# Kernel tuning notes

Hardware: AMD Instinct MI355X
Metric: run time of the kernel (lower is better)

## Reference

```python
import jax, jax.numpy as jnp
import numpy as np

DIM = 10  # GMM components == feature dim


def _conv(x, w, b):
    y = jax.lax.conv_general_dilated(x, w, window_strides=(1, 1), padding='VALID',
                                     dimension_numbers=('NCHW', 'OIHW', 'NCHW'))
    return y + b[None, :, None, None]


def _gmm(x, centers, raw_mats):
    # x: [B, d]; centers: [K, d]; raw_mats: [K, d, d] with K == d == DIM
    K, d = centers.shape
    I = jnp.eye(d, dtype=x.dtype)
    L = jnp.tril(raw_mats, -1) + I                       # unit lower-triangular [K,d,d]
    root_D = jnp.diagonal(raw_mats, axis1=-2, axis2=-1)  # [K,d]
    D = root_D * root_D + 1e-4
    # Sigma_inv = L^{-T} D^{-1} L^{-1}
    L_inv = jax.scipy.linalg.solve_triangular(L, jnp.broadcast_to(I, L.shape), lower=True)
    Sigma_inv = jnp.einsum('kai,ka,kaj->kij', L_inv, 1.0 / D, L_inv)
    det_scale = jax.lax.rsqrt(jnp.prod(D, axis=-1))      # [K]
    diff = x[:, None, :] - centers[None, :, :]           # [B,K,d]
    dist_sq = jnp.einsum('bkd,kde,bke->bk', diff, Sigma_inv, diff)
    expo = -0.5 * dist_sq
    expo_safe = expo - jnp.max(expo, axis=1, keepdims=True)
    numer = det_scale[None, :] * jnp.exp(expo_safe)
    return numer / jnp.sum(numer, axis=1, keepdims=True)


def setup_inputs() -> dict:
    key = jax.random.key(0)
    ks = jax.random.split(key, 12)
    B = 4096
    x = jax.random.normal(ks[0], (B, 1, 28, 28), dtype=jnp.float32)
    conv1_w = jax.random.normal(ks[1], (32, 1, 3, 3), jnp.float32) * (1.0 / np.sqrt(1 * 9))
    conv1_b = jnp.zeros((32,), jnp.float32)
    conv2_w = jax.random.normal(ks[2], (64, 32, 3, 3), jnp.float32) * (1.0 / np.sqrt(32 * 9))
    conv2_b = jnp.zeros((64,), jnp.float32)
    fc1_w = jax.random.normal(ks[3], (128, 9216), jnp.float32) * (1.0 / np.sqrt(9216))
    fc1_b = jnp.zeros((128,), jnp.float32)
    fc2_w = jax.random.normal(ks[4], (DIM, 128), jnp.float32) * (1.0 / np.sqrt(128))
    fc2_b = jnp.zeros((DIM,), jnp.float32)
    centers = jax.random.normal(ks[5], (DIM, DIM), jnp.float32)
    raw_mats = jax.random.normal(ks[6], (DIM, DIM, DIM), jnp.float32) * 0.1 + jnp.eye(DIM)[None]
    return {'x': x, 'conv1_w': conv1_w, 'conv1_b': conv1_b, 'conv2_w': conv2_w,
            'conv2_b': conv2_b, 'fc1_w': fc1_w, 'fc1_b': fc1_b, 'fc2_w': fc2_w,
            'fc2_b': fc2_b, 'centers': centers, 'raw_mats': raw_mats}


def reference(x, conv1_w, conv1_b, conv2_w, conv2_b, fc1_w, fc1_b, fc2_w, fc2_b, centers, raw_mats):
    h = jax.nn.relu(_conv(x, conv1_w, conv1_b))          # [B,32,26,26]
    h = jax.nn.relu(_conv(h, conv2_w, conv2_b))          # [B,64,24,24]
    h = jax.lax.reduce_window(h, -jnp.inf, jax.lax.max, (1, 1, 2, 2), (1, 1, 2, 2), 'VALID')
    h = h.reshape(h.shape[0], -1)                        # [B,9216] (dropout = identity in eval)
    h = jax.nn.relu(h @ fc1_w.T + fc1_b)
    h = h @ fc2_w.T + fc2_b                              # [B,10]
    return _gmm(h, centers, raw_mats)
```

## Files before the change

kernel.cpp:

```cpp
#include <hip/hip_runtime.h>

typedef _Float16 half_t;
typedef _Float16 half8  __attribute__((ext_vector_type(8)));
typedef _Float16 half2v __attribute__((ext_vector_type(2)));
typedef float    floatx4 __attribute__((ext_vector_type(4)));

#define MFMA16(a, b, c) __builtin_amdgcn_mfma_f32_16x16x32_f16((a), (b), (c), 0, 0, 0)

__global__ void k_prep(const float* __restrict__ fw1, half_t* __restrict__ W1h,
                       const float* __restrict__ w2, half_t* __restrict__ W2T,
                       const float* __restrict__ raw, float* __restrict__ Sinv,
                       float* __restrict__ dets) {
    const int blk = blockIdx.x;
    const int t = threadIdx.x;
    if (blk < 4608) {
        const int i = blk * 256 + t;
        W1h[i] = (half_t)fw1[i];
    } else if (blk < 4680) {
        const int i = (blk - 4608) * 256 + t;
        if (i < 18432) {
            const int tap = i / 2048;
            const int r = i - tap * 2048;
            const int co = r >> 5;
            const int ci = r & 31;
            W2T[i] = (half_t)w2[(co * 32 + ci) * 9 + tap];
        }
    } else if (t < 10) {
        const float* R = raw + t * 100;
        float Rr[100];
#pragma unroll
        for (int i = 0; i < 100; ++i) Rr[i] = R[i];
        float Li[10][10];
#pragma unroll
        for (int j = 0; j < 10; ++j) {
#pragma unroll
            for (int i = 0; i < 10; ++i) Li[i][j] = (i == j) ? 1.0f : 0.0f;
#pragma unroll
            for (int i = 1; i < 10; ++i) {
                if (i > j) {
                    float s = 0.0f;
#pragma unroll
                    for (int m = 0; m < 10; ++m)
                        if (m >= j && m < i) s -= Rr[i * 10 + m] * Li[m][j];
                    Li[i][j] = s;
                }
            }
        }
        float Dl[10];
        float prod = 1.0f;
#pragma unroll
        for (int a = 0; a < 10; ++a) {
            float rd = Rr[a * 10 + a];
            float dv = rd * rd + 1e-4f;
            Dl[a] = 1.0f / dv;
            prod *= dv;
        }
        dets[t] = rsqrtf(prod);
#pragma unroll
        for (int i = 0; i < 10; ++i)
#pragma unroll
            for (int j = 0; j < 10; ++j) {
                float s = 0.0f;
#pragma unroll
                for (int a = 0; a < 10; ++a) s += Li[a][i] * Dl[a] * Li[a][j];
                Sinv[t * 100 + i * 10 + j] = s;
            }
    }
}

__global__ __launch_bounds__(256, 2) void k_convs(
    const float* __restrict__ x, const float* __restrict__ w1,
    const float* __restrict__ b1, const float* __restrict__ b2,
    const half_t* __restrict__ W2T, half_t* __restrict__ h2p) {
    __shared__ float s_x[784];
    __shared__ float s_w1[288];
    __shared__ float s_b1[32];
    __shared__ float s_b2[64];
    __shared__ __align__(16) half_t s_h1[4][26][26][8];

    const int t = threadIdx.x;
    const int b = blockIdx.x;

    for (int i = t; i < 784; i += 256) s_x[i] = x[(size_t)b * 784 + i];
    for (int i = t; i < 288; i += 256) s_w1[i] = w1[i];
    if (t < 32) s_b1[t] = b1[t];
    if (t < 64) s_b2[t] = b2[t];
    __syncthreads();

    const int w = t >> 6;
    const int ln = t & 63;
    const int n16 = ln & 15;
    const int q = ln >> 4;

    {
        float wr[8][9], br[8];
#pragma unroll
        for (int j = 0; j < 8; ++j) {
            br[j] = s_b1[w * 8 + j];
#pragma unroll
            for (int k = 0; k < 9; ++k) wr[j][k] = s_w1[(w * 8 + j) * 9 + k];
        }
        for (int p = ln; p < 676; p += 64) {
            const int yy = p / 26;
            const int xx = p - yy * 26;
            float win[9];
#pragma unroll
            for (int r = 0; r < 3; ++r)
#pragma unroll
                for (int c = 0; c < 3; ++c) win[r * 3 + c] = s_x[(yy + r) * 28 + xx + c];
            half8 hv;
#pragma unroll
            for (int j = 0; j < 8; ++j) {
                float a = br[j];
#pragma unroll
                for (int k = 0; k < 9; ++k) a = fmaf(win[k], wr[j][k], a);
                hv[j] = (half_t)fmaxf(a, 0.0f);
            }
            *(half8*)(&s_h1[w][yy][xx][0]) = hv;
        }
    }

    half8 bf[9][4];
#pragma unroll
    for (int tap = 0; tap < 9; ++tap)
#pragma unroll
        for (int ct = 0; ct < 4; ++ct)
            bf[tap][ct] = *(const half8*)(W2T + ((tap * 64 + ct * 16 + n16) * 32 + q * 8));

    __syncthreads();

#pragma unroll
    for (int tap = 0; tap < 9; ++tap)
#pragma unroll
        for (int ct = 0; ct < 4; ++ct)
            asm volatile("" : "+v"(bf[tap][ct]));

    const int dy = (ln >> 3) & 1;
    const int dx = ln & 7;

    for (int i = 0; i < 9; ++i) {
        const int mt = w * 9 + i;
        const int ty = mt / 3;
        const int tx = mt - ty * 3;
        const int y0 = 2 * ty, x0 = 8 * tx;
        floatx4 acc[4];
#pragma unroll
        for (int ct = 0; ct < 4; ++ct) acc[ct] = (floatx4){0.f, 0.f, 0.f, 0.f};
#pragma unroll
        for (int tap = 0; tap < 9; ++tap) {
            const int ky = tap / 3;
            const int kx = tap - ky * 3;
            half8 af = *(const half8*)(&s_h1[q][y0 + dy + ky][x0 + dx + kx][0]);
#pragma unroll
            for (int ct = 0; ct < 4; ++ct) acc[ct] = MFMA16(af, bf[tap][ct], acc[ct]);
        }
#pragma unroll
        for (int ct = 0; ct < 4; ++ct) {
            float p0 = fmaxf(acc[ct][0], acc[ct][1]);
            float p1 = fmaxf(acc[ct][2], acc[ct][3]);
            p0 = fmaxf(p0, __shfl_xor(p0, 32, 64));
            p1 = fmaxf(p1, __shfl_xor(p1, 32, 64));
            if (q < 2) {
                const int co = ct * 16 + n16;
                const float bb = s_b2[co];
                half2v hz;
                hz[0] = (half_t)fmaxf(p0 + bb, 0.0f);
                hz[1] = (half_t)fmaxf(p1 + bb, 0.0f);
                *(half2v*)(h2p + (size_t)b * 9216 + co * 144 + ty * 12 + 4 * tx + 2 * q) = hz;
            }
        }
    }
}

__global__ __launch_bounds__(256) void k_fc1(const half_t* __restrict__ A,
                                             const half_t* __restrict__ W,
                                             half_t* __restrict__ part) {
    const int t = threadIdx.x;
    const int mb = blockIdx.x;
    const int kb = blockIdx.y;
    const int w = t >> 6, ln = t & 63, n16 = ln & 15, q = ln >> 4;

    const half_t* a0 = A + (size_t)(mb * 128 + w * 32 + n16) * 9216 + kb * 576 + q * 8;
    const half_t* a1 = a0 + (size_t)16 * 9216;
    const half_t* wp = W + (size_t)n16 * 9216 + kb * 576 + q * 8;

    floatx4 acc[2][8];
#pragma unroll
    for (int s = 0; s < 2; ++s)
#pragma unroll
        for (int nt = 0; nt < 8; ++nt) acc[s][nt] = (floatx4){0.f, 0.f, 0.f, 0.f};

    for (int kt = 0; kt < 18; ++kt) {
        const int ko = kt * 32;
        half8 af0 = *(const half8*)(a0 + ko);
        half8 af1 = *(const half8*)(a1 + ko);
#pragma unroll
        for (int nt = 0; nt < 8; ++nt) {
            half8 bfr = *(const half8*)(wp + (size_t)nt * 16 * 9216 + ko);
            acc[0][nt] = MFMA16(af0, bfr, acc[0][nt]);
            acc[1][nt] = MFMA16(af1, bfr, acc[1][nt]);
        }
    }
    const int rowbase = mb * 128 + w * 32;
#pragma unroll
    for (int s = 0; s < 2; ++s)
#pragma unroll
        for (int nt = 0; nt < 8; ++nt)
#pragma unroll
            for (int r = 0; r < 4; ++r) {
                const int row = rowbase + s * 16 + q * 4 + r;
                const int col = nt * 16 + n16;
                part[(size_t)kb * 524288 + (size_t)row * 128 + col] = (half_t)acc[s][nt][r];
            }
}

__global__ void k_fc1red(const half_t* __restrict__ part, const float* __restrict__ b,
                         half_t* __restrict__ h3) {
    const int idx = blockIdx.x * 256 + threadIdx.x;
    const int col = idx & 127;
    float s = 0.0f;
#pragma unroll
    for (int j = 0; j < 16; ++j) s += (float)part[(size_t)j * 524288 + idx];
    s = fmaxf(s + b[col], 0.0f);
    h3[idx] = (half_t)s;
}

__global__ __launch_bounds__(256) void k_fc2gmm(
    const half_t* __restrict__ h3, const float* __restrict__ fw,
    const float* __restrict__ fb, const float* __restrict__ cent,
    const float* __restrict__ Sinv, const float* __restrict__ dets,
    float* __restrict__ out) {
    __shared__ float sw[1280];
    __shared__ float sb[10];
    __shared__ float sc[100];
    __shared__ float ss[1000];
    __shared__ float sd[10];
    const int t = threadIdx.x;
    for (int i = t; i < 1280; i += 256) sw[i] = fw[i];
    if (t < 10) sb[t] = fb[t];
    if (t < 100) sc[t] = cent[t];
    for (int i = t; i < 1000; i += 256) ss[i] = Sinv[i];
    if (t < 10) sd[t] = dets[t];
    __syncthreads();

    const int bidx = blockIdx.x * 256 + t;
    half2v hh[64];
    const half2v* hp = (const half2v*)(h3 + (size_t)bidx * 128);
#pragma unroll
    for (int i = 0; i < 64; ++i) hh[i] = hp[i];

    float y[10];
#pragma unroll
    for (int o = 0; o < 10; ++o) {
        float a = sb[o];
#pragma unroll
        for (int k = 0; k < 64; ++k) {
            a = fmaf((float)hh[k][0], sw[o * 128 + 2 * k], a);
            a = fmaf((float)hh[k][1], sw[o * 128 + 2 * k + 1], a);
        }
        y[o] = a;
    }

    float expo[10];
    float mx = -3.402823466e38f;
#pragma unroll
    for (int k = 0; k < 10; ++k) {
        float d[10];
#pragma unroll
        for (int j = 0; j < 10; ++j) d[j] = y[j] - sc[k * 10 + j];
        float s = 0.0f;
#pragma unroll
        for (int i = 0; i < 10; ++i) {
            float r = 0.0f;
#pragma unroll
            for (int j = 0; j < 10; ++j) r = fmaf(ss[k * 100 + i * 10 + j], d[j], r);
            s = fmaf(d[i], r, s);
        }
        expo[k] = -0.5f * s;
        mx = fmaxf(mx, expo[k]);
    }
    float num[10];
    float sum = 0.0f;
#pragma unroll
    for (int k = 0; k < 10; ++k) {
        num[k] = sd[k] * __expf(expo[k] - mx);
        sum += num[k];
    }
    const float inv = 1.0f / sum;
#pragma unroll
    for (int k = 0; k < 10; ++k) out[(size_t)bidx * 10 + k] = num[k] * inv;
}

extern "C" void kernel_launch(void* const* d_in, const int* in_sizes, int n_in,
                              void* d_out, int out_size, void* d_ws, size_t ws_size,
                              hipStream_t stream) {
    const float* x = (const float*)d_in[0];
    const float* w1 = (const float*)d_in[1];
    const float* b1 = (const float*)d_in[2];
    const float* w2 = (const float*)d_in[3];
    const float* b2 = (const float*)d_in[4];
    const float* fw1 = (const float*)d_in[5];
    const float* fb1 = (const float*)d_in[6];
    const float* fw2 = (const float*)d_in[7];
    const float* fb2 = (const float*)d_in[8];
    const float* cen = (const float*)d_in[9];
    const float* raw = (const float*)d_in[10];
    float* out = (float*)d_out;

    char* ws = (char*)d_ws;
    half_t* W2T = (half_t*)(ws);
    half_t* W1h = (half_t*)(ws + 36864);
    half_t* h2p = (half_t*)(ws + 2396160);
    half_t* part = (half_t*)(ws + 77893632);
    half_t* h3h = (half_t*)(ws + 94670848);
    float* gS = (float*)(ws + 95719424);
    float* gD = (float*)(ws + 95723424);

    k_prep<<<4681, 256, 0, stream>>>(fw1, W1h, w2, W2T, raw, gS, gD);
    k_convs<<<4096, 256, 0, stream>>>(x, w1, b1, b2, W2T, h2p);
    k_fc1<<<dim3(32, 16), 256, 0, stream>>>(h2p, W1h, part);
    k_fc1red<<<2048, 256, 0, stream>>>(part, fb1, h3h);
    k_fc2gmm<<<16, 256, 0, stream>>>(h3h, fw2, fb2, cen, gS, gD, out);
}
```

Baseline: 283.6 us.

## Swizzle conv1 LDS layout, split conv2 channels across waves, parallelize GMM prep

The conv1 output in LDS becomes pixel-major with an XOR swizzle to reduce bank conflicts. Conv2 now splits output channels across wave pairs, so each wave holds half the B fragments. The M-tile mapping is changed so the 2x2 pool fits inside one accumulator's four elements, which removes the cross-lane shuffle. Launch bounds rise to 3 blocks per CU. The GMM precompute now spreads the triangular solve and Sigma_inv product over 100+ threads via shared memory instead of 10 serial threads. Output stores become scalar half writes, which may hurt coalescing.

Measured after the change: 261.2 us. 7.9% less time.

```diff
diff --git a/kernel.cpp b/kernel.cpp
--- a/kernel.cpp
+++ b/kernel.cpp
@@ -11,6 +11,9 @@
                        const float* __restrict__ w2, half_t* __restrict__ W2T,
                        const float* __restrict__ raw, float* __restrict__ Sinv,
                        float* __restrict__ dets) {
+    __shared__ float s_raw[1000];
+    __shared__ float s_Li[1000];
+    __shared__ float s_Dinv[100];
     const int blk = blockIdx.x;
     const int t = threadIdx.x;
     if (blk < 4608) {
@@ -25,50 +28,52 @@
             const int ci = r & 31;
             W2T[i] = (half_t)w2[(co * 32 + ci) * 9 + tap];
         }
-    } else if (t < 10) {
-        const float* R = raw + t * 100;
-        float Rr[100];
-#pragma unroll
-        for (int i = 0; i < 100; ++i) Rr[i] = R[i];
-        float Li[10][10];
-#pragma unroll
-        for (int j = 0; j < 10; ++j) {
-#pragma unroll
-            for (int i = 0; i < 10; ++i) Li[i][j] = (i == j) ? 1.0f : 0.0f;
-#pragma unroll
-            for (int i = 1; i < 10; ++i) {
-                if (i > j) {
-                    float s = 0.0f;
-#pragma unroll
-                    for (int m = 0; m < 10; ++m)
-                        if (m >= j && m < i) s -= Rr[i * 10 + m] * Li[m][j];
-                    Li[i][j] = s;
-                }
+    } else {
+        for (int i = t; i < 1000; i += 256) s_raw[i] = raw[i];
+        __syncthreads();
+        if (t < 100) {
+            const int k = t / 10;
+            const int j = t - k * 10;
+            float v[10];
+#pragma unroll
+            for (int i = 0; i < 10; ++i) {
+                float s = (i == j) ? 1.0f : 0.0f;
+#pragma unroll
+                for (int mm = 0; mm < 10; ++mm)
+                    if (mm < i) s -= s_raw[k * 100 + i * 10 + mm] * v[mm];
+                v[i] = s;
             }
-        }
-        float Dl[10];
-        float prod = 1.0f;
-#pragma unroll
-        for (int a = 0; a < 10; ++a) {
-            float rd = Rr[a * 10 + a];
-            float dv = rd * rd + 1e-4f;
-            Dl[a] = 1.0f / dv;
-            prod *= dv;
-        }
-        dets[t] = rsqrtf(prod);
-#pragma unroll
-        for (int i = 0; i < 10; ++i)
-#pragma unroll
-            for (int j = 0; j < 10; ++j) {
-                float s = 0.0f;
-#pragma unroll
-                for (int a = 0; a < 10; ++a) s += Li[a][i] * Dl[a] * Li[a][j];
-                Sinv[t * 100 + i * 10 + j] = s;
+#pragma unroll
+            for (int a = 0; a < 10; ++a) s_Li[k * 100 + a * 10 + j] = v[a];
+        } else if (t < 110) {
+            const int k = t - 100;
+            float prod = 1.0f;
+#pragma unroll
+            for (int a = 0; a < 10; ++a) {
+                const float rd = s_raw[k * 100 + a * 10 + a];
+                const float dv = rd * rd + 1e-4f;
+                s_Dinv[k * 10 + a] = 1.0f / dv;
+                prod *= dv;
             }
-    }
-}
-
-__global__ __launch_bounds__(256, 2) void k_convs(
+            dets[k] = rsqrtf(prod);
+        }
+        __syncthreads();
+        for (int idx = t; idx < 1000; idx += 256) {
+            const int k = idx / 100;
+            const int r = idx - k * 100;
+            const int ii = r / 10;
+            const int jj = r - ii * 10;
+            float s = 0.0f;
+#pragma unroll
+            for (int a = 0; a < 10; ++a)
+                s += s_Li[k * 100 + a * 10 + ii] * s_Dinv[k * 10 + a] *
+                     s_Li[k * 100 + a * 10 + jj];
+            Sinv[idx] = s;
+        }
+    }
+}
+
+__global__ __launch_bounds__(256, 3) void k_convs(
     const float* __restrict__ x, const float* __restrict__ w1,
     const float* __restrict__ b1, const float* __restrict__ b2,
     const half_t* __restrict__ W2T, half_t* __restrict__ h2p) {
@@ -76,7 +81,7 @@
     __shared__ float s_w1[288];
     __shared__ float s_b1[32];
     __shared__ float s_b2[64];
-    __shared__ __align__(16) half_t s_h1[4][26][26][8];
+    __shared__ __align__(16) half_t s_h1[21632];
 
     const int t = threadIdx.x;
     const int b = blockIdx.x;
@@ -116,59 +121,62 @@
                 for (int k = 0; k < 9; ++k) a = fmaf(win[k], wr[j][k], a);
                 hv[j] = (half_t)fmaxf(a, 0.0f);
             }
-            *(half8*)(&s_h1[w][yy][xx][0]) = hv;
-        }
-    }
-
-    half8 bf[9][4];
+            const int off = ((p << 6) + (w << 4)) ^ ((p & 7) << 4);
+            *(half8*)((char*)s_h1 + off) = hv;
+        }
+    }
+
+    const int cp = w & 1;
+    half8 bf[9][2];
 #pragma unroll
     for (int tap = 0; tap < 9; ++tap)
 #pragma unroll
-        for (int ct = 0; ct < 4; ++ct)
-            bf[tap][ct] = *(const half8*)(W2T + ((tap * 64 + ct * 16 + n16) * 32 + q * 8));
+        for (int cc = 0; cc < 2; ++cc)
+            bf[tap][cc] = *(const half8*)(W2T +
+                ((tap * 64 + (2 * cp + cc) * 16 + n16) * 32 + q * 8));
 
     __syncthreads();
 
 #pragma unroll
     for (int tap = 0; tap < 9; ++tap)
 #pragma unroll
-        for (int ct = 0; ct < 4; ++ct)
-            asm volatile("" : "+v"(bf[tap][ct]));
-
-    const int dy = (ln >> 3) & 1;
-    const int dx = ln & 7;
-
-    for (int i = 0; i < 9; ++i) {
-        const int mt = w * 9 + i;
-        const int ty = mt / 3;
-        const int tx = mt - ty * 3;
-        const int y0 = 2 * ty, x0 = 8 * tx;
-        floatx4 acc[4];
-#pragma unroll
-        for (int ct = 0; ct < 4; ++ct) acc[ct] = (floatx4){0.f, 0.f, 0.f, 0.f};
+        for (int cc = 0; cc < 2; ++cc)
+            asm volatile("" : "+v"(bf[tap][cc]));
+
+    const int am = ln & 15;
+    const int aly = 2 * ((am >> 2) & 1) + ((am >> 1) & 1);
+    const int alx = 2 * (am >> 3) + (am & 1);
+    const int qoff = q << 4;
+    const char* h1b = (const char*)s_h1;
+    const int mhalf = w >> 1;
+
+    for (int i = 0; i < 18; ++i) {
+        const int mt = mhalf * 18 + i;
+        const int tY = mt / 6;
+        const int tX = mt - tY * 6;
+        const int ybase = 4 * tY + aly;
+        const int xbase = 4 * tX + alx;
+        floatx4 acc0 = {0.f, 0.f, 0.f, 0.f};
+        floatx4 acc1 = {0.f, 0.f, 0.f, 0.f};
 #pragma unroll
         for (int tap = 0; tap < 9; ++tap) {
             const int ky = tap / 3;
             const int kx = tap - ky * 3;
-            half8 af = *(const half8*)(&s_h1[q][y0 + dy + ky][x0 + dx + kx][0]);
-#pragma unroll
-            for (int ct = 0; ct < 4; ++ct) acc[ct] = MFMA16(af, bf[tap][ct], acc[ct]);
-        }
-#pragma unroll
-        for (int ct = 0; ct < 4; ++ct) {
-            float p0 = fmaxf(acc[ct][0], acc[ct][1]);
-            float p1 = fmaxf(acc[ct][2], acc[ct][3]);
-            p0 = fmaxf(p0, __shfl_xor(p0, 32, 64));
-            p1 = fmaxf(p1, __shfl_xor(p1, 32, 64));
-            if (q < 2) {
-                const int co = ct * 16 + n16;
-                const float bb = s_b2[co];
-                half2v hz;
-                hz[0] = (half_t)fmaxf(p0 + bb, 0.0f);
-                hz[1] = (half_t)fmaxf(p1 + bb, 0.0f);
-                *(half2v*)(h2p + (size_t)b * 9216 + co * 144 + ty * 12 + 4 * tx + 2 * q) = hz;
-            }
-        }
+            const int pix = (ybase + ky) * 26 + xbase + kx;
+            const int off = ((pix << 6) + qoff) ^ ((pix & 7) << 4);
+            const half8 af = *(const half8*)(h1b + off);
+            acc0 = MFMA16(af, bf[tap][0], acc0);
+            acc1 = MFMA16(af, bf[tap][1], acc1);
+        }
+        const int poolY = 2 * tY + (q & 1);
+        const int poolX = 2 * tX + (q >> 1);
+        const float v0 = fmaxf(fmaxf(acc0[0], acc0[1]), fmaxf(acc0[2], acc0[3]));
+        const float v1 = fmaxf(fmaxf(acc1[0], acc1[1]), fmaxf(acc1[2], acc1[3]));
+        const int co0 = (2 * cp) * 16 + n16;
+        const int co1 = co0 + 16;
+        const size_t base = (size_t)b * 9216 + poolY * 12 + poolX;
+        h2p[base + (size_t)co0 * 144] = (half_t)fmaxf(v0 + s_b2[co0], 0.0f);
+        h2p[base + (size_t)co1 * 144] = (half_t)fmaxf(v1 + s_b2[co1], 0.0f);
     }
 }
 
```
